# Kernel tuning notes

Hardware: AMD Instinct MI355X
Metric: run time of the kernel (lower is better)

## Reference

```python
import jax, jax.numpy as jnp
import numpy as np

NUM_HEADS = 12

def setup_inputs() -> dict:
    key = jax.random.key(0)
    k1, k2, k3 = jax.random.split(key, 3)
    B, N, D = 16, 1024, 768
    x = jax.random.normal(k1, (B, N, D), dtype=jnp.float32)
    w_qkv = jax.random.normal(k2, (D, 3 * D), dtype=jnp.float32) * (D ** -0.5)
    b_qkv = jnp.zeros((3 * D,), dtype=jnp.float32)
    w_proj = jax.random.normal(k3, (D, D), dtype=jnp.float32) * (D ** -0.5)
    b_proj = jnp.zeros((D,), dtype=jnp.float32)
    return {"x": x, "w_qkv": w_qkv, "b_qkv": b_qkv, "w_proj": w_proj, "b_proj": b_proj}

def reference(x, w_qkv, b_qkv, w_proj, b_proj):
    B, N, D = x.shape
    H = NUM_HEADS
    Hd = D // H
    scale = Hd ** -0.5
    qkv = x @ w_qkv + b_qkv                       # (B, N, 3D)
    qkv = qkv.reshape(B, N, 3, H, Hd)
    q, k, v = qkv[:, :, 0], qkv[:, :, 1], qkv[:, :, 2]  # (B, N, H, Hd)
    attn = jnp.einsum('bnhd,bmhd->bhnm', q, k) * scale  # (B, H, N, N)
    attn = jax.nn.softmax(attn, axis=-1)
    out = jnp.einsum('bhnm,bmhd->bnhd', attn, v).reshape(B, N, D)
    return out @ w_proj + b_proj
```

## Files before the change

### kernel.cpp

```cpp
#include <hip/hip_runtime.h>


typedef _Float16 half8 __attribute__((ext_vector_type(8)));
typedef _Float16 half4 __attribute__((ext_vector_type(4)));
typedef __fp16   fp16x2 __attribute__((ext_vector_type(2)));
typedef float    f32x4  __attribute__((ext_vector_type(4)));
typedef float    f32x16 __attribute__((ext_vector_type(16)));
typedef unsigned int u32x4 __attribute__((ext_vector_type(4)));

#define DI __device__ __forceinline__

constexpr int   BATCH  = 16;
constexpr int   SEQ    = 1024;
constexpr int   DM     = 768;
constexpr int   NH     = 12;
constexpr int   HD     = 64;
constexpr float SCALE  = 0.125f;
constexpr float LOG2E  = 1.4426950408889634f;

DI void copy16(_Float16* dst, const _Float16* src) {
  *(u32x4*)dst = *(const u32x4*)src;
}

DI int pack_rtz(float a, float b) {
  union { fp16x2 h; int i; } u;
  u.h = __builtin_amdgcn_cvt_pkrtz(a, b);
  return u.i;
}

DI void gld16(const _Float16* g, _Float16* l) {
  __builtin_amdgcn_global_load_lds(
      (const __attribute__((address_space(1))) void*)g,
      (__attribute__((address_space(3))) void*)l, 16, 0, 0);
}

__global__ void cvt_x_kernel(const float* __restrict__ x,
                             _Float16* __restrict__ xh, int n4) {
  int i = blockIdx.x * 256 + threadIdx.x;
  if (i >= n4) return;
  float4 v = ((const float4*)x)[i];
  half4 h;
  h[0] = (_Float16)v.x; h[1] = (_Float16)v.y;
  h[2] = (_Float16)v.z; h[3] = (_Float16)v.w;
  *(half4*)(xh + (size_t)i * 4) = h;
}

__global__ void cvt_wt2_kernel(const float* __restrict__ wq,
                               _Float16* __restrict__ wqT,
                               const float* __restrict__ wp,
                               _Float16* __restrict__ wpT) {
  __shared__ float tile[32][33];
  const int by = blockIdx.y;
  const float* w; _Float16* wt; int N, nb;
  if (by < 72) { w = wq; wt = wqT; N = 2304; nb = by * 32; }
  else         { w = wp; wt = wpT; N = 768;  nb = (by - 72) * 32; }
  const int K = 768;
  int kb = blockIdx.x * 32;
  int tx = threadIdx.x & 31, ty = threadIdx.x >> 5;
#pragma unroll
  for (int i = 0; i < 32; i += 8)
    tile[ty + i][tx] = w[(size_t)(kb + ty + i) * N + nb + tx];
  __syncthreads();
#pragma unroll
  for (int i = 0; i < 32; i += 8)
    wt[(size_t)(nb + ty + i) * K + kb + tx] = (_Float16)tile[tx][ty + i];
}

__launch_bounds__(256, 3)
__global__ void gemm_qkv_kernel(const _Float16* __restrict__ A,
                                const _Float16* __restrict__ Bt,
                                const float* __restrict__ bias,
                                _Float16* __restrict__ Qo,
                                _Float16* __restrict__ Ko,
                                _Float16* __restrict__ VTo) {
  __shared__ _Float16 sh[16384];
  _Float16* Cs = sh;
  const int tid  = threadIdx.x;
  const int lin  = blockIdx.x;
  const int xcd  = lin & 7, j = lin >> 3;
  const int ct   = j % 18;
  const int m0   = ((j / 18) * 8 + xcd) * 128;
  const int n0   = ct * 128;
  const int w    = tid >> 6, lane = tid & 63;
  const int quad = lane >> 4, l15 = lane & 15;
  const int wr   = w >> 1, wc = w & 1;

  f32x4 acc[4][4] = {};

  const int g0 = tid + w * 64;
  const int r0 = g0 >> 2, s0 = g0 & 3;
  const _Float16* gaA = A  + (size_t)(m0 + r0) * 768 + s0 * 8;
  const _Float16* gaB = Bt + (size_t)(n0 + r0) * 768 + s0 * 8;
  const int ldst = w * 1024;

  auto STAGE = [&](int buf, int kt) {
    _Float16* As = sh + buf * 8192;
    _Float16* Bs = As + 4096;
    const _Float16* a = gaA + kt * 32;
    const _Float16* b = gaB + kt * 32;
    gld16(a,            As + ldst);
    gld16(a + 16 * 768, As + ldst + 512);
    gld16(b,            Bs + ldst);
    gld16(b + 16 * 768, Bs + ldst + 512);
  };

  STAGE(0, 0);

  for (int kt = 0; kt < 24; ++kt) {
    __syncthreads();
    if (kt < 23) STAGE((kt + 1) & 1, kt + 1);

    const _Float16* As = sh + (kt & 1) * 8192;
    const _Float16* Bs = As + 4096;

    half8 af[4], bf[4];
#pragma unroll
    for (int mi = 0; mi < 4; mi++)
      af[mi] = *(const half8*)&As[(wr * 64 + mi * 16 + l15) * 32 + quad * 8];
#pragma unroll
    for (int ni = 0; ni < 4; ni++)
      bf[ni] = *(const half8*)&Bs[(wc * 64 + ni * 16 + l15) * 32 + quad * 8];
#pragma unroll
    for (int mi = 0; mi < 4; mi++)
#pragma unroll
      for (int ni = 0; ni < 4; ni++)
        acc[mi][ni] = __builtin_amdgcn_mfma_f32_16x16x32_f16(
            af[mi], bf[ni], acc[mi][ni], 0, 0, 0);
  }
  __syncthreads();

  const float oscale = (ct < 6) ? SCALE : 1.0f;
  float bcol[4];
#pragma unroll
  for (int ni = 0; ni < 4; ni++)
    bcol[ni] = bias[n0 + wc * 64 + ni * 16 + l15];

  const int b     = m0 >> 10;
  const int nrow0 = m0 & 1023;
  const int sec   = ct / 6;
  const int h0    = (ct % 6) * 2;

#pragma unroll
  for (int p = 0; p < 2; ++p) {
    if (p) __syncthreads();
    if (wr == p) {
#pragma unroll
      for (int mi = 0; mi < 4; mi++)
#pragma unroll
        for (int ni = 0; ni < 4; ni++) {
          int col = wc * 64 + ni * 16 + l15;
          int row = mi * 16 + quad * 4;
#pragma unroll
          for (int r = 0; r < 4; r++)
            Cs[(row + r) * 136 + col] =
                (_Float16)((acc[mi][ni][r] + bcol[ni]) * oscale);
        }
    }
    __syncthreads();

    if (sec < 2) {
      _Float16* dst = (sec == 0) ? Qo : Ko;
      int row = tid >> 2, seg = tid & 3;
      int hl = seg >> 1, off32 = (seg & 1) * 32;
      _Float16* g = dst +
          ((size_t)((b * NH + h0 + hl) * SEQ + nrow0 + p * 64 + row)) * HD + off32;
      const _Float16* s = &Cs[row * 136 + hl * 64 + off32];
      copy16(g, s);
      copy16(g + 8, s + 8);
      copy16(g + 16, s + 16);
      copy16(g + 24, s + 24);
    } else {
      int c = tid & 127, half = tid >> 7;
      int hl = c >> 6, d = c & 63;
      _Float16 tmp[32];
#pragma unroll
      for (int jj = 0; jj < 32; jj++) tmp[jj] = Cs[(half * 32 + jj) * 136 + c];
      _Float16* g = VTo + ((size_t)((b * NH + h0 + hl) * HD + d)) * SEQ
                        + nrow0 + p * 64 + half * 32;
#pragma unroll
      for (int jj = 0; jj < 4; jj++)
        copy16(g + jj * 8, (const _Float16*)&tmp[jj * 8]);
    }
  }
}

__launch_bounds__(256, 2)
__global__ void attn_kernel(const _Float16* __restrict__ Q,
                            const _Float16* __restrict__ K,
                            const _Float16* __restrict__ VT,
                            _Float16* __restrict__ Oh) {
  __shared__ _Float16 smem[2][2][64 * 72];
  _Float16* OLds = &smem[0][0][0];

  const int tid = threadIdx.x;
  const int i   = blockIdx.x;
  const int bh  = (i & 7) * 24 + ((i >> 3) >> 2);
  const int q0  = ((i >> 3) & 3) * 256;
  const int b   = bh / NH, hh = bh - b * NH;
  const int w   = tid >> 6, lane = tid & 63;
  const int l31 = lane & 31, h = lane >> 5;

  const _Float16* Qg = Q  + (size_t)bh * SEQ * HD;
  const _Float16* Kg = K  + (size_t)bh * SEQ * HD;
  const _Float16* Vg = VT + (size_t)bh * HD * SEQ;

  half8 qb[2][4];
#pragma unroll
  for (int N = 0; N < 2; N++) {
    const _Float16* qrow = Qg + (size_t)(q0 + w * 64 + N * 32 + l31) * HD + h * 8;
#pragma unroll
    for (int s = 0; s < 4; s++)
      qb[N][s] = *(const half8*)(qrow + s * 16);
  }

  const int  sr  = (tid & 127) >> 1;
  const int  sp  = tid & 1;
  const bool isK = tid < 128;
  const _Float16* sg = isK ? (Kg + sr * HD + sp * 32)
                           : (Vg + (size_t)sr * SEQ + sp * 32);
  const int sstep = isK ? 64 * HD : 64;
  const int soff  = (isK ? 0 : 64 * 72) + sr * 72 + sp * 32;

  u32x4 pf[4];
#pragma unroll
  for (int c = 0; c < 4; c++) pf[c] = *(const u32x4*)(sg + c * 8);
#pragma unroll
  for (int c = 0; c < 4; c++) *(u32x4*)(&smem[0][0][0] + soff + c * 8) = pf[c];

  f32x16 of[2][2];
#pragma unroll
  for (int D = 0; D < 2; D++)
#pragma unroll
    for (int N = 0; N < 2; N++)
#pragma unroll
      for (int r = 0; r < 16; r++) of[D][N][r] = 0.f;
  float m_[2] = {-1e30f, -1e30f}, l_[2] = {0.f, 0.f};

  for (int kt = 0; kt < 16; ++kt) {
    if (kt < 15) {
      const _Float16* nsg = sg + (kt + 1) * sstep;
#pragma unroll
      for (int c = 0; c < 4; c++) pf[c] = *(const u32x4*)(nsg + c * 8);
    }
    __syncthreads();
    const _Float16* Ks = &smem[kt & 1][0][0];
    const _Float16* Vs = &smem[kt & 1][1][0];

    f32x16 sf[2][2];
#pragma unroll
    for (int M = 0; M < 2; M++)
#pragma unroll
      for (int N = 0; N < 2; N++)
#pragma unroll
        for (int r = 0; r < 16; r++) sf[M][N][r] = 0.f;
#pragma unroll
    for (int s = 0; s < 4; s++) {
      half8 ka0 = *(const half8*)&Ks[l31 * 72 + s * 16 + h * 8];
      half8 ka1 = *(const half8*)&Ks[(32 + l31) * 72 + s * 16 + h * 8];
#pragma unroll
      for (int N = 0; N < 2; N++) {
        sf[0][N] = __builtin_amdgcn_mfma_f32_32x32x16_f16(ka0, qb[N][s], sf[0][N], 0, 0, 0);
        sf[1][N] = __builtin_amdgcn_mfma_f32_32x32x16_f16(ka1, qb[N][s], sf[1][N], 0, 0, 0);
      }
    }

    float alpha[2], c1[2], tsum[2];
#pragma unroll
    for (int N = 0; N < 2; N++) {
      float tmax = -1e30f;
#pragma unroll
      for (int r = 0; r < 16; r++)
        tmax = fmaxf(tmax, fmaxf(sf[0][N][r], sf[1][N][r]));
      tmax = fmaxf(tmax, __shfl_xor(tmax, 32, 64));
      float mnew = fmaxf(m_[N], tmax);
      alpha[N] = __builtin_amdgcn_exp2f((m_[N] - mnew) * LOG2E);
      m_[N] = mnew;
      c1[N] = mnew * LOG2E;
      tsum[N] = 0.f;
    }

    int pdw[2][2][8];
#pragma unroll
    for (int M = 0; M < 2; M++)
#pragma unroll
      for (int N = 0; N < 2; N++) {
#pragma unroll
        for (int r = 0; r < 16; r++) {
          float p = __builtin_amdgcn_exp2f(sf[M][N][r] * LOG2E - c1[N]);
          sf[M][N][r] = p;
          tsum[N] += p;
        }
#pragma unroll
        for (int u = 0; u < 8; u++)
          pdw[M][N][u] = pack_rtz(sf[M][N][2 * u], sf[M][N][2 * u + 1]);
      }
#pragma unroll
    for (int N = 0; N < 2; N++) {
      tsum[N] += __shfl_xor(tsum[N], 32, 64);
      l_[N] = l_[N] * alpha[N] + tsum[N];
    }
#pragma unroll
    for (int D = 0; D < 2; D++)
#pragma unroll
      for (int N = 0; N < 2; N++)
#pragma unroll
        for (int r = 0; r < 16; r++) of[D][N][r] *= alpha[N];

#pragma unroll
    for (int t = 0; t < 4; ++t) {
      const int M = t >> 1, s2 = (t & 1) * 4;
      half8 va0 = *(const half8*)&Vs[l31 * 72 + t * 16 + h * 8];
      half8 va1 = *(const half8*)&Vs[(32 + l31) * 72 + t * 16 + h * 8];
#pragma unroll
      for (int N = 0; N < 2; N++) {
        int a0 = pdw[M][N][s2 + 0], a1 = pdw[M][N][s2 + 1];
        int a2 = pdw[M][N][s2 + 2], a3 = pdw[M][N][s2 + 3];
        int e0 = h ? a0 : a2, e1 = h ? a1 : a3;
        int r0 = __shfl_xor(e0, 32, 64), r1 = __shfl_xor(e1, 32, 64);
        union { u32x4 u; half8 hv; } bb;
        bb.u[0] = h ? r0 : a0; bb.u[1] = h ? r1 : a1;
        bb.u[2] = h ? a2 : r0; bb.u[3] = h ? a3 : r1;
        of[0][N] = __builtin_amdgcn_mfma_f32_32x32x16_f16(va0, bb.hv, of[0][N], 0, 0, 0);
        of[1][N] = __builtin_amdgcn_mfma_f32_32x32x16_f16(va1, bb.hv, of[1][N], 0, 0, 0);
      }
    }

    if (kt < 15) {
      _Float16* dst = &smem[(kt + 1) & 1][0][0] + soff;
#pragma unroll
      for (int c = 0; c < 4; c++) *(u32x4*)(dst + c * 8) = pf[c];
    }
  }

  __syncthreads();
  float inv[2] = {1.0f / l_[0], 1.0f / l_[1]};
  int* OW = (int*)OLds;
#pragma unroll
  for (int N = 0; N < 2; N++) {
    const int q_local = w * 64 + N * 32 + l31;
#pragma unroll
    for (int D = 0; D < 2; D++)
#pragma unroll
      for (int u = 0; u < 8; u++) {
        int v = pack_rtz(of[D][N][2 * u] * inv[N], of[D][N][2 * u + 1] * inv[N]);
        int dwi = 16 * D + 4 * (u >> 1) + (u & 1) + 2 * h;
        OW[q_local * 36 + dwi] = v;
      }
  }
  __syncthreads();
#pragma unroll
  for (int p = 0; p < 8; p++) {
    int q = p * 32 + (tid >> 3), c = tid & 7;
    *(u32x4*)(Oh + (size_t)(b * SEQ + q0 + q) * DM + hh * HD + c * 8) =
        *(const u32x4*)&OLds[q * 72 + c * 8];
  }
}

__launch_bounds__(256, 3)
__global__ void gemm_proj_kernel(const _Float16* __restrict__ A,
                                 const _Float16* __restrict__ Bt,
                                 const float* __restrict__ bias,
                                 float* __restrict__ out) {
  __shared__ _Float16 sh[16384];
  const int tid  = threadIdx.x;
  const int lin  = blockIdx.x;
  const int xcd  = lin & 7, j = lin >> 3;
  const int ct   = j % 6;
  const int m0   = ((j / 6) * 8 + xcd) * 128;
  const int n0   = ct * 128;
  const int w    = tid >> 6, lane = tid & 63;
  const int quad = lane >> 4, l15 = lane & 15;
  const int wr   = w >> 1, wc = w & 1;

  f32x4 acc[4][4] = {};

  const int g0 = tid + w * 64;
  const int r0 = g0 >> 2, s0 = g0 & 3;
  const _Float16* gaA = A  + (size_t)(m0 + r0) * 768 + s0 * 8;
  const _Float16* gaB = Bt + (size_t)(n0 + r0) * 768 + s0 * 8;
  const int ldst = w * 1024;

  auto STAGE = [&](int buf, int kt) {
    _Float16* As = sh + buf * 8192;
    _Float16* Bs = As + 4096;
    const _Float16* a = gaA + kt * 32;
    const _Float16* b = gaB + kt * 32;
    gld16(a,            As + ldst);
    gld16(a + 16 * 768, As + ldst + 512);
    gld16(b,            Bs + ldst);
    gld16(b + 16 * 768, Bs + ldst + 512);
  };

  STAGE(0, 0);

  for (int kt = 0; kt < 24; ++kt) {
    __syncthreads();
    if (kt < 23) STAGE((kt + 1) & 1, kt + 1);

    const _Float16* As = sh + (kt & 1) * 8192;
    const _Float16* Bs = As + 4096;

    half8 af[4], bf[4];
#pragma unroll
    for (int mi = 0; mi < 4; mi++)
      af[mi] = *(const half8*)&As[(wr * 64 + mi * 16 + l15) * 32 + quad * 8];
#pragma unroll
    for (int ni = 0; ni < 4; ni++)
      bf[ni] = *(const half8*)&Bs[(wc * 64 + ni * 16 + l15) * 32 + quad * 8];
#pragma unroll
    for (int mi = 0; mi < 4; mi++)
#pragma unroll
      for (int ni = 0; ni < 4; ni++)
        acc[mi][ni] = __builtin_amdgcn_mfma_f32_16x16x32_f16(
            af[mi], bf[ni], acc[mi][ni], 0, 0, 0);
  }

  float bcol[4];
#pragma unroll
  for (int ni = 0; ni < 4; ni++)
    bcol[ni] = bias[n0 + wc * 64 + ni * 16 + l15];
#pragma unroll
  for (int mi = 0; mi < 4; mi++)
#pragma unroll
    for (int ni = 0; ni < 4; ni++) {
      int col = n0 + wc * 64 + ni * 16 + l15;
      int row = m0 + wr * 64 + mi * 16 + quad * 4;
#pragma unroll
      for (int r = 0; r < 4; r++)
        out[(size_t)(row + r) * 768 + col] = acc[mi][ni][r] + bcol[ni];
    }
}

extern "C" void kernel_launch(void* const* d_in, const int* in_sizes, int n_in,
                              void* d_out, int out_size, void* d_ws, size_t ws_size,
                              hipStream_t stream) {
  const float* x      = (const float*)d_in[0];
  const float* w_qkv  = (const float*)d_in[1];
  const float* b_qkv  = (const float*)d_in[2];
  const float* w_proj = (const float*)d_in[3];
  const float* b_proj = (const float*)d_in[4];
  float* out = (float*)d_out;

  char* ws = (char*)d_ws;
  _Float16* xh     = (_Float16*)(ws);
  _Float16* wqkvT  = (_Float16*)(ws + 25165824);
  _Float16* wprojT = (_Float16*)(ws + 28704768);
  _Float16* Qp     = (_Float16*)(ws + 29884416);
  _Float16* Kp     = (_Float16*)(ws + 55050240);
  _Float16* VTp    = (_Float16*)(ws + 80216064);
  _Float16* Ohp    = (_Float16*)(ws + 105381888);

  cvt_x_kernel<<<dim3(3145728 / 256), 256, 0, stream>>>(x, xh, 3145728);
  cvt_wt2_kernel<<<dim3(24, 96), 256, 0, stream>>>(w_qkv, wqkvT, w_proj, wprojT);
  gemm_qkv_kernel<<<dim3(2304), 256, 0, stream>>>(xh, wqkvT, b_qkv, Qp, Kp, VTp);
  attn_kernel<<<dim3(768), 256, 0, stream>>>(Qp, Kp, VTp, Ohp);
  gemm_proj_kernel<<<dim3(768), 256, 0, stream>>>(Ohp, wprojT, b_proj, out);
}
```

Measured before the change: 311.2 us.

## Enlarge GEMM tiles to 256x256 with 4-stage swizzled LDS pipeline

Both the QKV and projection GEMMs move from 128x128 tiles with 256 threads to 256x256 tiles with 512 threads, sharing a new core routine. The routine uses a 4-deep global-to-LDS prefetch with explicit vmcnt waits, XOR-swizzled LDS columns to avoid bank conflicts, split A-half loads interleaved with MFMA phases, and s_setprio around the MFMA blocks. The aim is more operand reuse per loaded byte and better overlap of loads with compute. In exchange, the grids get much smaller (576 and 192 blocks), which may underfill the GPU's CUs, and register pressure rises with 32 accumulators per thread.

```diff
diff --git a/kernel.cpp b/kernel.cpp
--- a/kernel.cpp
+++ b/kernel.cpp
@@ -32,6 +32,12 @@
   __builtin_amdgcn_global_load_lds(
       (const __attribute__((address_space(1))) void*)g,
       (__attribute__((address_space(3))) void*)l, 16, 0, 0);
+}
+
+DI void wg_barrier() {
+  asm volatile("" ::: "memory");
+  __builtin_amdgcn_s_barrier();
+  asm volatile("" ::: "memory");
 }
 
 __global__ void cvt_x_kernel(const float* __restrict__ x,
@@ -66,93 +72,135 @@
     wt[(size_t)(nb + ty + i) * K + kb + tx] = (_Float16)tile[tx][ty + i];
 }
 
-__launch_bounds__(256, 3)
+constexpr int ABUFH = 8192;
+constexpr int BREG  = 32768;
+constexpr int KT    = 24;
+
+DI void gemm256_core(const _Float16* __restrict__ A,
+                     const _Float16* __restrict__ Bt,
+                     _Float16* sh, int m0, int n0,
+                     f32x4 (&acc)[8][4]) {
+  const int tid  = threadIdx.x;
+  const int wv   = tid >> 6, lane = tid & 63;
+  const int quad = lane >> 4, l15 = lane & 15;
+  const int wr   = wv >> 2,  wc  = wv & 3;
+
+  const int srow = wv * 32 + (lane >> 2);
+  const int scol = ((lane & 3) ^ (2 * ((lane >> 5) & 1))) * 8;
+  const _Float16* sA = A  + (size_t)(m0 + srow) * 768 + scol;
+  const _Float16* sB = Bt + (size_t)(n0 + srow) * 768 + scol;
+  const int sd = wv * 1024;
+
+  auto stageA = [&](int kt) {
+    const _Float16* s = sA + kt * 32;
+    _Float16* d = sh + (kt & 3) * ABUFH + sd;
+    gld16(s, d);
+    gld16(s + 16 * 768, d + 512);
+  };
+  auto stageB = [&](int kt) {
+    const _Float16* s = sB + kt * 32;
+    _Float16* d = sh + BREG + (kt & 3) * ABUFH + sd;
+    gld16(s, d);
+    gld16(s + 16 * 768, d + 512);
+  };
+
+  const int qa   = (quad ^ (2 * ((l15 >> 3) & 1))) * 8;
+  const int aoff = (wr * 128 + l15) * 32 + qa;
+  const int boff = BREG + (wc * 64 + l15) * 32 + qa;
+
+  stageA(0); stageB(0); stageA(1); stageB(1); stageA(2); stageB(2);
+  asm volatile("s_waitcnt vmcnt(8)" ::: "memory");
+  wg_barrier();
+
+  for (int kt = 0; kt < KT; ++kt) {
+    const int bufo = (kt & 3) * ABUFH;
+    const _Float16* Ab = sh + bufo + aoff;
+    const _Float16* Bb = sh + bufo + boff;
+    half8 af[4], bf[4];
+#pragma unroll
+    for (int mi = 0; mi < 4; ++mi) af[mi] = *(const half8*)(Ab + mi * 512);
+#pragma unroll
+    for (int ni = 0; ni < 4; ++ni) bf[ni] = *(const half8*)(Bb + ni * 512);
+    if (kt + 3 < KT) stageA(kt + 3);
+    wg_barrier();
+    asm volatile("s_waitcnt lgkmcnt(0)" ::: "memory");
+    __builtin_amdgcn_s_setprio(1);
+#pragma unroll
+    for (int mi = 0; mi < 4; ++mi)
+#pragma unroll
+      for (int ni = 0; ni < 4; ++ni)
+        acc[mi][ni] = __builtin_amdgcn_mfma_f32_16x16x32_f16(
+            af[mi], bf[ni], acc[mi][ni], 0, 0, 0);
+    __builtin_amdgcn_s_setprio(0);
+    wg_barrier();
+    half8 ag[4];
+#pragma unroll
+    for (int mi = 0; mi < 4; ++mi) ag[mi] = *(const half8*)(Ab + 2048 + mi * 512);
+    if (kt + 3 < KT) stageB(kt + 3);
+    wg_barrier();
+    asm volatile("s_waitcnt lgkmcnt(0)" ::: "memory");
+    __builtin_amdgcn_s_setprio(1);
+#pragma unroll
+    for (int mi = 0; mi < 4; ++mi)
+#pragma unroll
+      for (int ni = 0; ni < 4; ++ni)
+        acc[4 + mi][ni] = __builtin_amdgcn_mfma_f32_16x16x32_f16(
+            ag[mi], bf[ni], acc[4 + mi][ni], 0, 0, 0);
+    __builtin_amdgcn_s_setprio(0);
+    if (kt < 21)       asm volatile("s_waitcnt vmcnt(8)" ::: "memory");
+    else if (kt == 21) asm volatile("s_waitcnt vmcnt(4)" ::: "memory");
+    else if (kt == 22) asm volatile("s_waitcnt vmcnt(0)" ::: "memory");
+    wg_barrier();
+  }
+}
+
+__launch_bounds__(512, 2)
 __global__ void gemm_qkv_kernel(const _Float16* __restrict__ A,
                                 const _Float16* __restrict__ Bt,
                                 const float* __restrict__ bias,
                                 _Float16* __restrict__ Qo,
                                 _Float16* __restrict__ Ko,
                                 _Float16* __restrict__ VTo) {
-  __shared__ _Float16 sh[16384];
+  __shared__ _Float16 sh[65536];
+  const int lin = blockIdx.x;
+  const int xcd = lin & 7, j = lin >> 3;
+  const int ct  = j % 9;
+  const int m0  = ((j / 9) * 8 + xcd) * 256;
+  const int n0  = ct * 256;
+
+  f32x4 acc[8][4] = {};
+  gemm256_core(A, Bt, sh, m0, n0, acc);
+  __syncthreads();
+
+  const int tid  = threadIdx.x;
+  const int wv   = tid >> 6, lane = tid & 63;
+  const int quad = lane >> 4, l15 = lane & 15;
+  const int wr   = wv >> 2,  wc  = wv & 3;
+
+  const int   sec    = ct / 3;
+  const int   h0     = (ct % 3) * 4;
+  const float oscale = (sec == 0) ? SCALE : 1.0f;
+  float bcol[4];
+#pragma unroll
+  for (int ni = 0; ni < 4; ++ni)
+    bcol[ni] = bias[n0 + wc * 64 + ni * 16 + l15];
+
+  const int b = m0 >> 10, nrow0 = m0 & 1023;
   _Float16* Cs = sh;
-  const int tid  = threadIdx.x;
-  const int lin  = blockIdx.x;
-  const int xcd  = lin & 7, j = lin >> 3;
-  const int ct   = j % 18;
-  const int m0   = ((j / 18) * 8 + xcd) * 128;
-  const int n0   = ct * 128;
-  const int w    = tid >> 6, lane = tid & 63;
-  const int quad = lane >> 4, l15 = lane & 15;
-  const int wr   = w >> 1, wc = w & 1;
-
-  f32x4 acc[4][4] = {};
-
-  const int g0 = tid + w * 64;
-  const int r0 = g0 >> 2, s0 = g0 & 3;
-  const _Float16* gaA = A  + (size_t)(m0 + r0) * 768 + s0 * 8;
-  const _Float16* gaB = Bt + (size_t)(n0 + r0) * 768 + s0 * 8;
-  const int ldst = w * 1024;
-
-  auto STAGE = [&](int buf, int kt) {
-    _Float16* As = sh + buf * 8192;
-    _Float16* Bs = As + 4096;
-    const _Float16* a = gaA + kt * 32;
-    const _Float16* b = gaB + kt * 32;
-    gld16(a,            As + ldst);
-    gld16(a + 16 * 768, As + ldst + 512);
-    gld16(b,            Bs + ldst);
-    gld16(b + 16 * 768, Bs + ldst + 512);
-  };
-
-  STAGE(0, 0);
-
-  for (int kt = 0; kt < 24; ++kt) {
-    __syncthreads();
-    if (kt < 23) STAGE((kt + 1) & 1, kt + 1);
-
-    const _Float16* As = sh + (kt & 1) * 8192;
-    const _Float16* Bs = As + 4096;
-
-    half8 af[4], bf[4];
-#pragma unroll
-    for (int mi = 0; mi < 4; mi++)
-      af[mi] = *(const half8*)&As[(wr * 64 + mi * 16 + l15) * 32 + quad * 8];
-#pragma unroll
-    for (int ni = 0; ni < 4; ni++)
-      bf[ni] = *(const half8*)&Bs[(wc * 64 + ni * 16 + l15) * 32 + quad * 8];
-#pragma unroll
-    for (int mi = 0; mi < 4; mi++)
-#pragma unroll
-      for (int ni = 0; ni < 4; ni++)
-        acc[mi][ni] = __builtin_amdgcn_mfma_f32_16x16x32_f16(
-            af[mi], bf[ni], acc[mi][ni], 0, 0, 0);
-  }
-  __syncthreads();
-
-  const float oscale = (ct < 6) ? SCALE : 1.0f;
-  float bcol[4];
-#pragma unroll
-  for (int ni = 0; ni < 4; ni++)
-    bcol[ni] = bias[n0 + wc * 64 + ni * 16 + l15];
-
-  const int b     = m0 >> 10;
-  const int nrow0 = m0 & 1023;
-  const int sec   = ct / 6;
-  const int h0    = (ct % 6) * 2;
 
 #pragma unroll
   for (int p = 0; p < 2; ++p) {
     if (p) __syncthreads();
     if (wr == p) {
 #pragma unroll
-      for (int mi = 0; mi < 4; mi++)
-#pragma unroll
-        for (int ni = 0; ni < 4; ni++) {
-          int col = wc * 64 + ni * 16 + l15;
-          int row = mi * 16 + quad * 4;
-#pragma unroll
-          for (int r = 0; r < 4; r++)
-            Cs[(row + r) * 136 + col] =
+      for (int mi = 0; mi < 8; ++mi)
+#pragma unroll
+        for (int ni = 0; ni < 4; ++ni) {
+          int lr = mi * 16 + quad * 4;
+          int lc = wc * 64 + ni * 16 + l15;
+#pragma unroll
+          for (int r = 0; r < 4; ++r)
+            Cs[(lr + r) * 264 + lc] =
                 (_Float16)((acc[mi][ni][r] + bcol[ni]) * oscale);
         }
     }
@@ -161,25 +209,26 @@
     if (sec < 2) {
       _Float16* dst = (sec == 0) ? Qo : Ko;
       int row = tid >> 2, seg = tid & 3;
-      int hl = seg >> 1, off32 = (seg & 1) * 32;
       _Float16* g = dst +
-          ((size_t)((b * NH + h0 + hl) * SEQ + nrow0 + p * 64 + row)) * HD + off32;
-      const _Float16* s = &Cs[row * 136 + hl * 64 + off32];
-      copy16(g, s);
-      copy16(g + 8, s + 8);
-      copy16(g + 16, s + 16);
-      copy16(g + 24, s + 24);
+          ((size_t)((b * NH + h0 + seg) * SEQ + nrow0 + p * 128 + row)) * HD;
+      const _Float16* s = &Cs[row * 264 + seg * 64];
+#pragma unroll
+      for (int k2 = 0; k2 < 8; ++k2) copy16(g + k2 * 8, s + k2 * 8);
     } else {
-      int c = tid & 127, half = tid >> 7;
-      int hl = c >> 6, d = c & 63;
-      _Float16 tmp[32];
-#pragma unroll
-      for (int jj = 0; jj < 32; jj++) tmp[jj] = Cs[(half * 32 + jj) * 136 + c];
-      _Float16* g = VTo + ((size_t)((b * NH + h0 + hl) * HD + d)) * SEQ
-                        + nrow0 + p * 64 + half * 32;
-#pragma unroll
-      for (int jj = 0; jj < 4; jj++)
-        copy16(g + jj * 8, (const _Float16*)&tmp[jj * 8]);
+      int c = tid & 255, rh = tid >> 8;
+      _Float16* g = VTo +
+          ((size_t)((b * NH + h0 + (c >> 6)) * HD + (c & 63))) * SEQ +
+          nrow0 + p * 128 + rh * 64;
+#pragma unroll
+      for (int ch = 0; ch < 2; ++ch) {
+        _Float16 tmp[32];
+#pragma unroll
+        for (int jj = 0; jj < 32; ++jj)
+          tmp[jj] = Cs[(rh * 64 + ch * 32 + jj) * 264 + c];
+#pragma unroll
+        for (int k2 = 0; k2 < 4; ++k2)
+          copy16(g + ch * 32 + k2 * 8, (const _Float16*)&tmp[k2 * 8]);
+      }
     }
   }
 }
@@ -356,77 +405,38 @@
   }
 }
 
-__launch_bounds__(256, 3)
+__launch_bounds__(512, 2)
 __global__ void gemm_proj_kernel(const _Float16* __restrict__ A,
                                  const _Float16* __restrict__ Bt,
                                  const float* __restrict__ bias,
                                  float* __restrict__ out) {
-  __shared__ _Float16 sh[16384];
+  __shared__ _Float16 sh[65536];
+  const int lin = blockIdx.x;
+  const int xcd = lin & 7, j = lin >> 3;
+  const int ct  = j % 3;
+  const int m0  = ((j / 3) * 8 + xcd) * 256;
+  const int n0  = ct * 256;
+
+  f32x4 acc[8][4] = {};
+  gemm256_core(A, Bt, sh, m0, n0, acc);
+
   const int tid  = threadIdx.x;
-  const int lin  = blockIdx.x;
-  const int xcd  = lin & 7, j = lin >> 3;
-  const int ct   = j % 6;
-  const int m0   = ((j / 6) * 8 + xcd) * 128;
-  const int n0   = ct * 128;
-  const int w    = tid >> 6, lane = tid & 63;
+  const int wv   = tid >> 6, lane = tid & 63;
   const int quad = lane >> 4, l15 = lane & 15;
-  const int wr   = w >> 1, wc = w & 1;
-
-  f32x4 acc[4][4] = {};
-
-  const int g0 = tid + w * 64;
-  const int r0 = g0 >> 2, s0 = g0 & 3;
-  const _Float16* gaA = A  + (size_t)(m0 + r0) * 768 + s0 * 8;
-  const _Float16* gaB = Bt + (size_t)(n0 + r0) * 768 + s0 * 8;
-  const int ldst = w * 1024;
-
-  auto STAGE = [&](int buf, int kt) {
-    _Float16* As = sh + buf * 8192;
-    _Float16* Bs = As + 4096;
-    const _Float16* a = gaA + kt * 32;
-    const _Float16* b = gaB + kt * 32;
-    gld16(a,            As + ldst);
-    gld16(a + 16 * 768, As + ldst + 512);
-    gld16(b,            Bs + ldst);
-    gld16(b + 16 * 768, Bs + ldst + 512);
-  };
-
-  STAGE(0, 0);
-
-  for (int kt = 0; kt < 24; ++kt) {
-    __syncthreads();
-    if (kt < 23) STAGE((kt + 1) & 1, kt + 1);
-
-    const _Float16* As = sh + (kt & 1) * 8192;
-    const _Float16* Bs = As + 4096;
-
-    half8 af[4], bf[4];
-#pragma unroll
-    for (int mi = 0; mi < 4; mi++)
-      af[mi] = *(const half8*)&As[(wr * 64 + mi * 16 + l15) * 32 + quad * 8];
-#pragma unroll
-    for (int ni = 0; ni < 4; ni++)
-      bf[ni] = *(const half8*)&Bs[(wc * 64 + ni * 16 + l15) * 32 + quad * 8];
-#pragma unroll
-    for (int mi = 0; mi < 4; mi++)
-#pragma unroll
-      for (int ni = 0; ni < 4; ni++)
-        acc[mi][ni] = __builtin_amdgcn_mfma_f32_16x16x32_f16(
-            af[mi], bf[ni], acc[mi][ni], 0, 0, 0);
-  }
+  const int wr   = wv >> 2,  wc  = wv & 3;
 
   float bcol[4];
 #pragma unroll
-  for (int ni = 0; ni < 4; ni++)
+  for (int ni = 0; ni < 4; ++ni)
     bcol[ni] = bias[n0 + wc * 64 + ni * 16 + l15];
 #pragma unroll
-  for (int mi = 0; mi < 4; mi++)
-#pragma unroll
-    for (int ni = 0; ni < 4; ni++) {
+  for (int mi = 0; mi < 8; ++mi)
+#pragma unroll
+    for (int ni = 0; ni < 4; ++ni) {
       int col = n0 + wc * 64 + ni * 16 + l15;
-      int row = m0 + wr * 64 + mi * 16 + quad * 4;
-#pragma unroll
-      for (int r = 0; r < 4; r++)
+      int row = m0 + wr * 128 + mi * 16 + quad * 4;
+#pragma unroll
+      for (int r = 0; r < 4; ++r)
         out[(size_t)(row + r) * 768 + col] = acc[mi][ni][r] + bcol[ni];
     }
 }
@@ -452,7 +462,7 @@
 
   cvt_x_kernel<<<dim3(3145728 / 256), 256, 0, stream>>>(x, xh, 3145728);
   cvt_wt2_kernel<<<dim3(24, 96), 256, 0, stream>>>(w_qkv, wqkvT, w_proj, wprojT);
-  gemm_qkv_kernel<<<dim3(2304), 256, 0, stream>>>(xh, wqkvT, b_qkv, Qp, Kp, VTp);
+  gemm_qkv_kernel<<<dim3(576), 512, 0, stream>>>(xh, wqkvT, b_qkv, Qp, Kp, VTp);
   attn_kernel<<<dim3(768), 256, 0, stream>>>(Qp, Kp, VTp, Ohp);
-  gemm_proj_kernel<<<dim3(768), 256, 0, stream>>>(Ohp, wprojT, b_proj, out);
-}
+  gemm_proj_kernel<<<dim3(192), 512, 0, stream>>>(Ohp, wprojT, b_proj, out);
+}
```

Result: slower. 318.2 us (+2.3%).

## Skip online-softmax rescale when max grows little; raise priority around MFMA blocks

Applied to the files above, without the earlier changes.

Adds a lazy rescale to the flash-attention loop: the running max and the accumulator/denominator rescaling are updated only when some row's tile max exceeds the stored max by more than a threshold, checked wave-wide. This avoids the per-tile alpha exp and the 64-element accumulator multiply in most iterations, at the cost of letting exponents reach up to 2^(8*log2e), which stays within fp16 range for P. It also wraps the QK and PV MFMA blocks in s_setprio so waves issuing matrix work are favoured over the softmax phase of other waves.

```diff
diff --git a/kernel.cpp b/kernel.cpp
--- a/kernel.cpp
+++ b/kernel.cpp
@@ -253,6 +253,7 @@
       for (int N = 0; N < 2; N++)
 #pragma unroll
         for (int r = 0; r < 16; r++) sf[M][N][r] = 0.f;
+    __builtin_amdgcn_s_setprio(1);
 #pragma unroll
     for (int s = 0; s < 4; s++) {
       half8 ka0 = *(const half8*)&Ks[l31 * 72 + s * 16 + h * 8];
@@ -263,21 +264,34 @@
         sf[1][N] = __builtin_amdgcn_mfma_f32_32x32x16_f16(ka1, qb[N][s], sf[1][N], 0, 0, 0);
       }
     }
-
-    float alpha[2], c1[2], tsum[2];
+    __builtin_amdgcn_s_setprio(0);
+
+    float tmax[2];
 #pragma unroll
     for (int N = 0; N < 2; N++) {
-      float tmax = -1e30f;
+      float tm = -1e30f;
 #pragma unroll
       for (int r = 0; r < 16; r++)
-        tmax = fmaxf(tmax, fmaxf(sf[0][N][r], sf[1][N][r]));
-      tmax = fmaxf(tmax, __shfl_xor(tmax, 32, 64));
-      float mnew = fmaxf(m_[N], tmax);
-      alpha[N] = __builtin_amdgcn_exp2f((m_[N] - mnew) * LOG2E);
-      m_[N] = mnew;
-      c1[N] = mnew * LOG2E;
-      tsum[N] = 0.f;
-    }
+        tm = fmaxf(tm, fmaxf(sf[0][N][r], sf[1][N][r]));
+      tm = fmaxf(tm, __shfl_xor(tm, 32, 64));
+      tmax[N] = tm;
+    }
+    if (!__all((tmax[0] <= m_[0] + 8.f) && (tmax[1] <= m_[1] + 8.f))) {
+#pragma unroll
+      for (int N = 0; N < 2; N++) {
+        float mnew  = fmaxf(m_[N], tmax[N]);
+        float alpha = __builtin_amdgcn_exp2f((m_[N] - mnew) * LOG2E);
+        m_[N] = mnew;
+        l_[N] *= alpha;
+#pragma unroll
+        for (int D = 0; D < 2; D++)
+#pragma unroll
+          for (int r = 0; r < 16; r++) of[D][N][r] *= alpha;
+      }
+    }
+    float c1[2], tsum[2];
+#pragma unroll
+    for (int N = 0; N < 2; N++) { c1[N] = m_[N] * LOG2E; tsum[N] = 0.f; }
 
     int pdw[2][2][8];
 #pragma unroll
@@ -297,15 +311,10 @@
 #pragma unroll
     for (int N = 0; N < 2; N++) {
       tsum[N] += __shfl_xor(tsum[N], 32, 64);
-      l_[N] = l_[N] * alpha[N] + tsum[N];
-    }
-#pragma unroll
-    for (int D = 0; D < 2; D++)
-#pragma unroll
-      for (int N = 0; N < 2; N++)
-#pragma unroll
-        for (int r = 0; r < 16; r++) of[D][N][r] *= alpha[N];
-
+      l_[N] += tsum[N];
+    }
+
+    __builtin_amdgcn_s_setprio(1);
 #pragma unroll
     for (int t = 0; t < 4; ++t) {
       const int M = t >> 1, s2 = (t & 1) * 4;
@@ -324,6 +333,7 @@
         of[1][N] = __builtin_amdgcn_mfma_f32_32x32x16_f16(va1, bb.hv, of[1][N], 0, 0, 0);
       }
     }
+    __builtin_amdgcn_s_setprio(0);
 
     if (kt < 15) {
       _Float16* dst = &smem[(kt + 1) & 1][0][0] + soff;
```

Measured after the change: 314.2 us. No clear change (+1.0%).
